# Optimization experiments

Hardware: AMD Instinct MI355X
Metric: run time of the kernel (lower is better)

Reference implementation:

```python
import jax, jax.numpy as jnp
import numpy as np

D_MODEL = 128
H = 256          # lstm_hidden_dim
L = 2            # lstm_num_layers
PRED_LEN = 45
OUT_DIM = 2
B = 4096


def _glorot(key, shape):
    fan = shape[-1]
    return jax.random.uniform(key, shape, jnp.float32, -1.0, 1.0) / jnp.sqrt(jnp.float32(fan))


def setup_inputs() -> dict:
    key = jax.random.key(0)
    ks = jax.random.split(key, 20)
    inp = {
        "encoder_feat": jax.random.normal(ks[0], (B, D_MODEL), jnp.float32),
        "last_obs_pos": jax.random.normal(ks[1], (B, OUT_DIM), jnp.float32),
        "context": jax.random.normal(ks[2], (B, D_MODEL), jnp.float32),
        # hidden/cell init projections: Linear(d_model -> H*L)
        "Wh_init": _glorot(ks[3], (H * L, D_MODEL)),
        "bh_init": jnp.zeros((H * L,), jnp.float32),
        "Wc_init": _glorot(ks[4], (H * L, D_MODEL)),
        "bc_init": jnp.zeros((H * L,), jnp.float32),
        # LSTM layer 0: input = OUT_DIM + D_MODEL
        "W_ih0": _glorot(ks[5], (4 * H, OUT_DIM + D_MODEL)),
        "W_hh0": _glorot(ks[6], (4 * H, H)),
        "b_ih0": jnp.zeros((4 * H,), jnp.float32),
        "b_hh0": jnp.zeros((4 * H,), jnp.float32),
        # LSTM layer 1: input = H
        "W_ih1": _glorot(ks[7], (4 * H, H)),
        "W_hh1": _glorot(ks[8], (4 * H, H)),
        "b_ih1": jnp.zeros((4 * H,), jnp.float32),
        "b_hh1": jnp.zeros((4 * H,), jnp.float32),
        # output_proj: Linear(H,64) -> ReLU -> Linear(64, OUT_DIM)
        "Wp1": _glorot(ks[9], (64, H)),
        "bp1": jnp.zeros((64,), jnp.float32),
        "Wp2": _glorot(ks[10], (OUT_DIM, 64)),
        "bp2": jnp.zeros((OUT_DIM,), jnp.float32),
    }
    return inp


def _lstm_cell(gates_x, h, c, W_hh):
    # gates_x already = x @ W_ih.T + b_ih + b_hh ; torch gate order: i, f, g, o
    gates = gates_x + h @ W_hh.T
    i, f, g, o = jnp.split(gates, 4, axis=-1)
    c_new = jax.nn.sigmoid(f) * c + jax.nn.sigmoid(i) * jnp.tanh(g)
    h_new = jax.nn.sigmoid(o) * jnp.tanh(c_new)
    return h_new, c_new


def reference(encoder_feat, last_obs_pos, context,
              Wh_init, bh_init, Wc_init, bc_init,
              W_ih0, W_hh0, b_ih0, b_hh0,
              W_ih1, W_hh1, b_ih1, b_hh1,
              Wp1, bp1, Wp2, bp2):
    b = encoder_feat.shape[0]
    # init hidden/cell: [B, L*H] -> per-layer [B, H]
    h_all = (encoder_feat @ Wh_init.T + bh_init).reshape(b, L, H)
    c_all = (encoder_feat @ Wc_init.T + bc_init).reshape(b, L, H)
    h0, h1 = h_all[:, 0], h_all[:, 1]
    c0, c1 = c_all[:, 0], c_all[:, 1]

    # context is constant across steps: precompute its gate contribution once
    bias0 = b_ih0 + b_hh0
    gates_ctx = context @ W_ih0[:, OUT_DIM:].T + bias0   # [B, 4H]
    W_pos = W_ih0[:, :OUT_DIM]                            # [4H, 2]
    bias1 = b_ih1 + b_hh1

    def step(carry, _):
        pos, h0, c0, h1, c1 = carry
        gates_x0 = gates_ctx + pos @ W_pos.T
        h0, c0 = _lstm_cell(gates_x0, h0, c0, W_hh0)
        gates_x1 = h0 @ W_ih1.T + bias1
        h1, c1 = _lstm_cell(gates_x1, h1, c1, W_hh1)
        delta = jax.nn.relu(h1 @ Wp1.T + bp1) @ Wp2.T + bp2
        pos = pos + delta
        return (pos, h0, c0, h1, c1), pos

    _, traj = jax.lax.scan(step, (last_obs_pos, h0, c0, h1, c1), None, length=PRED_LEN)
    return jnp.transpose(traj, (1, 0, 2))  # [B, pred_len, 2]
```

## Files before the change

kernel.cpp:

```cpp
#include <hip/hip_runtime.h>


#define HN    256
#define DM    128
#define NSTEP 45

#define H0A_OFF  1605632ULL
#define HBUF_B   2097152ULL
#define H0B_OFF  (H0A_OFF + HBUF_B)
#define H1A_OFF  (H0B_OFF + HBUF_B)
#define H1B_OFF  (H1A_OFF + HBUF_B)
#define GX_OFF   (H1B_OFF + HBUF_B)
#define GX_B     8388608ULL
#define C0_OFF   (GX_OFF + GX_B)
#define CB_B     4194304ULL
#define C1_OFF   (C0_OFF + CB_B)
#define POSA_OFF (C1_OFF + CB_B)
#define POSB_OFF (POSA_OFF + 32768ULL)
#define WS_NEED  (POSB_OFF + 32768ULL)

typedef __attribute__((ext_vector_type(8))) short s8v;
typedef __attribute__((ext_vector_type(4))) float f32x4;

#define MFMA16(a,b,c) __builtin_amdgcn_mfma_f32_16x16x32_bf16((a),(b),(c),0,0,0)

__device__ __forceinline__ unsigned short f2bf(float f){
  union { float f; unsigned u; } x; x.f = f;
  unsigned r = x.u + 0x7fffu + ((x.u >> 16) & 1u);
  return (unsigned short)(r >> 16);
}
__device__ __forceinline__ float bf2f(unsigned short h){
  union { unsigned u; float f; } x; x.u = ((unsigned)h) << 16;
  return x.f;
}
__device__ __forceinline__ float sigm(float x){
  x = fminf(40.f, fmaxf(-40.f, x));
  return 1.f/(1.f + __expf(-x));
}
__device__ __forceinline__ float tanhx(float x){
  float xx = fminf(15.f, fmaxf(-15.f, x));
  float e = __expf(2.f*xx);
  return (e-1.f)/(e+1.f);
}

__device__ __forceinline__ void store_h(unsigned short* buf, int blk, int b, int u, float v){
  buf[(size_t)blk*4096 + (u>>5)*512 + ((b&15) + ((u>>3)&3)*16)*8 + (u&7)] = f2bf(v);
}
__device__ __forceinline__ s8v ld_af(const unsigned short* buf, int blk, int kt, int lane){
  return *(const s8v*)(buf + (size_t)blk*4096 + kt*512 + lane*8);
}

__global__ void repack(const float* __restrict__ Whh0, const float* __restrict__ Wih1,
                       const float* __restrict__ Whh1, const float* __restrict__ Wp1,
                       unsigned short* __restrict__ dst){
  int gid  = blockIdx.x*256 + threadIdx.x;
  int lane = gid & 63;
  int tile = gid >> 6;
  const float* src; int row; size_t doff;
  int k0 = (lane>>4)*8;
  if (tile < 1536){
    int mi = tile / 512;
    int r  = tile % 512;
    int ut = r & 15;
    int kt = (r >> 4) & 7;
    int g  = r >> 7;
    src  = (mi==0) ? Whh0 : (mi==1) ? Wih1 : Whh1;
    row  = g*256 + ut*16 + (lane&15);
    k0  += kt*32;
    doff = (size_t)mi*262144 + (size_t)r*512 + lane*8;
  } else {
    int r2 = tile - 1536;
    int kt = r2 & 7, pt = r2 >> 3;
    src  = Wp1;
    row  = pt*16 + (lane&15);
    k0  += kt*32;
    doff = 786432 + (size_t)r2*512 + lane*8;
  }
  const float* s = src + (size_t)row*HN + k0;
  float4 a = *(const float4*)(s);
  float4 b = *(const float4*)(s+4);
  unsigned short* d = dst + doff;
  d[0]=f2bf(a.x); d[1]=f2bf(a.y); d[2]=f2bf(a.z); d[3]=f2bf(a.w);
  d[4]=f2bf(b.x); d[5]=f2bf(b.y); d[6]=f2bf(b.z); d[7]=f2bf(b.w);
}

__global__ __launch_bounds__(512, 1)
void k_init(const float* __restrict__ enc, const float* __restrict__ pos0,
            const float* __restrict__ ctx, const float* __restrict__ Wh,
            const float* __restrict__ bh,  const float* __restrict__ Wc,
            const float* __restrict__ bc,  const float* __restrict__ Wih0,
            const float* __restrict__ bih0,const float* __restrict__ bhh0,
            unsigned short* __restrict__ h0a, unsigned short* __restrict__ h1a,
            unsigned short* __restrict__ gxg,
            float* __restrict__ c0g, float* __restrict__ c1g,
            float* __restrict__ posg)
{
  __shared__ float sh_x[16*DM];
  const int tid = threadIdx.x;
  const int blk = blockIdx.x;
  const int gb0 = blk*16;

  {
    const float4* src = (const float4*)(enc + (size_t)gb0*DM);
    ((float4*)sh_x)[tid] = src[tid];
  }
  if (tid < 32) posg[(size_t)gb0*2 + tid] = pos0[(size_t)gb0*2 + tid];
  __syncthreads();

  {
    const int r = tid;
    float ah[16], ac[16];
    #pragma unroll
    for (int b=0;b<16;b++){ ah[b]=0.f; ac[b]=0.f; }
    const float4* whr = (const float4*)(Wh + (size_t)r*DM);
    const float4* wcr = (const float4*)(Wc + (size_t)r*DM);
    #pragma unroll 4
    for (int kk=0; kk<DM/4; kk++){
      float4 w0 = whr[kk], w1 = wcr[kk];
      #pragma unroll
      for (int b=0;b<16;b++){
        float4 x = *(const float4*)&sh_x[b*DM + kk*4];
        ah[b] += w0.x*x.x + w0.y*x.y + w0.z*x.z + w0.w*x.w;
        ac[b] += w1.x*x.x + w1.y*x.y + w1.z*x.z + w1.w*x.w;
      }
    }
    float bhv = bh[r], bcv = bc[r];
    if (r < HN){
      #pragma unroll
      for (int b=0;b<16;b++){
        store_h(h0a, blk, b, r, ah[b] + bhv);
        c0g[(size_t)blk*4096 + r*16 + b] = ac[b] + bcv;
      }
    } else {
      #pragma unroll
      for (int b=0;b<16;b++){
        store_h(h1a, blk, b, r-HN, ah[b] + bhv);
        c1g[(size_t)blk*4096 + (r-HN)*16 + b] = ac[b] + bcv;
      }
    }
  }
  __syncthreads();

  {
    const float4* src = (const float4*)(ctx + (size_t)gb0*DM);
    ((float4*)sh_x)[tid] = src[tid];
  }
  __syncthreads();

  {
    float a0[16], a1[16];
    #pragma unroll
    for (int b=0;b<16;b++){ a0[b]=0.f; a1[b]=0.f; }
    const float2* wr0 = (const float2*)(Wih0 + (size_t)tid*130 + 2);
    const float2* wr1 = (const float2*)(Wih0 + (size_t)(tid+512)*130 + 2);
    #pragma unroll 4
    for (int kk=0; kk<DM/2; kk++){
      float2 w0 = wr0[kk], w1 = wr1[kk];
      #pragma unroll
      for (int b=0;b<16;b++){
        float2 x = *(const float2*)&sh_x[b*DM + kk*2];
        a0[b] += w0.x*x.x + w0.y*x.y;
        a1[b] += w1.x*x.x + w1.y*x.y;
      }
    }
    float cb0 = bih0[tid]     + bhh0[tid];
    float cb1 = bih0[tid+512] + bhh0[tid+512];
    #pragma unroll
    for (int b=0;b<16;b++){
      gxg[(size_t)blk*16384 + (size_t)tid*16 + b]       = f2bf(a0[b] + cb0);
      gxg[(size_t)blk*16384 + (size_t)(tid+512)*16 + b] = f2bf(a1[b] + cb1);
    }
  }
}

__global__ __launch_bounds__(512, 1)
void k_layer0(const unsigned short* __restrict__ wsW,
              const unsigned short* __restrict__ gxg,
              const unsigned short* __restrict__ h0rd,
              unsigned short* __restrict__ h0wr,
              const unsigned short* __restrict__ h1prev,
              float* __restrict__ c0g,
              const float* __restrict__ posRd,
              float* __restrict__ posWr,
              const float* __restrict__ Wih0,
              const float* __restrict__ bp1,
              const float* __restrict__ Wp2,
              const float* __restrict__ bp2,
              float* __restrict__ out, int t)
{
  const int tid  = threadIdx.x;
  const int lane = tid & 63;
  const int w    = tid >> 6;
  const int wb   = w >> 1;
  const int wh   = w & 1;
  const int col  = lane & 15;
  const int hi   = lane >> 4;
  const int bt   = blockIdx.x & 31;
  const int sl   = blockIdx.x >> 5;

  const int blk0 = bt*8 + wb*2;
  const int ut   = sl*2 + wh;
  const int u    = ut*16 + col;

  f32x4 acc[2][4];
  #pragma unroll
  for (int m2=0;m2<2;m2++)
    #pragma unroll
    for (int g=0;g<4;g++)
      #pragma unroll
      for (int q=0;q<4;q++) acc[m2][g][q] = 0.f;

  float p0[2][4], p1[2][4];

  if (t > 0){
    float bpv[4], w2a[4], w2b[4];
    #pragma unroll
    for (int n=0;n<4;n++){
      bpv[n] = bp1[n*16 + col];
      w2a[n] = Wp2[n*16 + col];
      w2b[n] = Wp2[64 + n*16 + col];
    }
    f32x4 hp[2][4];
    #pragma unroll
    for (int m2=0;m2<2;m2++)
      #pragma unroll
      for (int n=0;n<4;n++)
        #pragma unroll
        for (int q=0;q<4;q++) hp[m2][n][q] = bpv[n];

    #pragma unroll
    for (int kt=0;kt<8;kt++){
      s8v a0 = ld_af(h0rd,   blk0,   kt, lane);
      s8v a1 = ld_af(h0rd,   blk0+1, kt, lane);
      s8v b0 = ld_af(h1prev, blk0,   kt, lane);
      s8v b1 = ld_af(h1prev, blk0+1, kt, lane);
      #pragma unroll
      for (int g=0;g<4;g++){
        const int r = (g*8 + kt)*16 + ut;
        s8v bf = *(const s8v*)(wsW + (size_t)r*512 + lane*8);
        acc[0][g] = MFMA16(a0, bf, acc[0][g]);
        acc[1][g] = MFMA16(a1, bf, acc[1][g]);
        s8v wf = *(const s8v*)(wsW + 786432 + (size_t)(g*8+kt)*512 + lane*8);
        hp[0][g] = MFMA16(b0, wf, hp[0][g]);
        hp[1][g] = MFMA16(b1, wf, hp[1][g]);
      }
    }

    const float bp20 = bp2[0], bp21 = bp2[1];
    #pragma unroll
    for (int m2=0;m2<2;m2++){
      const int blk = blk0 + m2;
      #pragma unroll
      for (int q=0;q<4;q++){
        float s0 = 0.f, s1 = 0.f;
        #pragma unroll
        for (int n=0;n<4;n++){
          float r = fmaxf(hp[m2][n][q], 0.f);
          s0 += r*w2a[n]; s1 += r*w2b[n];
        }
        #pragma unroll
        for (int off=1; off<16; off<<=1){
          s0 += __shfl_xor(s0, off, 64);
          s1 += __shfl_xor(s1, off, 64);
        }
        int b = blk*16 + hi*4 + q;
        float2 pp = *(const float2*)(posRd + (size_t)b*2);
        float np0 = pp.x + s0 + bp20;
        float np1 = pp.y + s1 + bp21;
        p0[m2][q] = np0; p1[m2][q] = np1;
        if (sl == 0 && wh == 0 && col == 0){
          posWr[(size_t)b*2]     = np0;
          posWr[(size_t)b*2 + 1] = np1;
          out[((size_t)b*NSTEP + (t-1))*2]     = np0;
          out[((size_t)b*NSTEP + (t-1))*2 + 1] = np1;
        }
      }
    }
  } else {
    #pragma unroll
    for (int kt=0;kt<8;kt++){
      s8v a0 = ld_af(h0rd, blk0,   kt, lane);
      s8v a1 = ld_af(h0rd, blk0+1, kt, lane);
      #pragma unroll
      for (int g=0;g<4;g++){
        const int r = (g*8 + kt)*16 + ut;
        s8v bf = *(const s8v*)(wsW + (size_t)r*512 + lane*8);
        acc[0][g] = MFMA16(a0, bf, acc[0][g]);
        acc[1][g] = MFMA16(a1, bf, acc[1][g]);
      }
    }
    #pragma unroll
    for (int m2=0;m2<2;m2++)
      #pragma unroll
      for (int q=0;q<4;q++){
        float2 pp = *(const float2*)(posRd + (size_t)((blk0+m2)*16 + hi*4 + q)*2);
        p0[m2][q] = pp.x; p1[m2][q] = pp.y;
      }
  }

  float wpr[4][2];
  #pragma unroll
  for (int g=0;g<4;g++){
    int row = g*256 + u;
    wpr[g][0] = Wih0[(size_t)row*130 + 0];
    wpr[g][1] = Wih0[(size_t)row*130 + 1];
  }
  #pragma unroll
  for (int m2=0;m2<2;m2++){
    const int blk = blk0 + m2;
    float* cp = c0g + (size_t)blk*4096 + u*16 + hi*4;
    float4 cold = *(const float4*)cp;
    float4 cnew;
    #pragma unroll
    for (int q=0;q<4;q++){
      float gate[4];
      #pragma unroll
      for (int g=0;g<4;g++){
        const unsigned short* gp = gxg + (size_t)blk*16384 + (size_t)(g*256+u)*16 + hi*4;
        gate[g] = acc[m2][g][q] + bf2f(gp[q]) + p0[m2][q]*wpr[g][0] + p1[m2][q]*wpr[g][1];
      }
      float iv = sigm(gate[0]);
      float fv = sigm(gate[1]);
      float gv = tanhx(gate[2]);
      float ov = sigm(gate[3]);
      float cv = fv*((&cold.x)[q]) + iv*gv;
      (&cnew.x)[q] = cv;
      store_h(h0wr, blk, hi*4+q, u, ov*tanhx(cv));
    }
    *(float4*)cp = cnew;
  }
}

__global__ __launch_bounds__(512, 1)
void k_layer1(const unsigned short* __restrict__ wsW,
              const unsigned short* __restrict__ h0n,
              const unsigned short* __restrict__ h1rd,
              unsigned short* __restrict__ h1wr,
              float* __restrict__ c1g,
              const float* __restrict__ bih1,
              const float* __restrict__ bhh1)
{
  const int tid  = threadIdx.x;
  const int lane = tid & 63;
  const int w    = tid >> 6;
  const int wb   = w >> 1;
  const int wh   = w & 1;
  const int col  = lane & 15;
  const int hi   = lane >> 4;
  const int bt   = blockIdx.x & 31;
  const int sl   = blockIdx.x >> 5;

  const int blk0 = bt*8 + wb*2;
  const int ut   = sl*2 + wh;
  const int u    = ut*16 + col;

  f32x4 acc[2][4];
  #pragma unroll
  for (int g=0;g<4;g++){
    int row = g*256 + u;
    float bv = bih1[row] + bhh1[row];
    #pragma unroll
    for (int q=0;q<4;q++){ acc[0][g][q] = bv; acc[1][g][q] = bv; }
  }

  #pragma unroll
  for (int kt=0;kt<8;kt++){
    s8v x0 = ld_af(h0n,  blk0,   kt, lane);
    s8v x1 = ld_af(h0n,  blk0+1, kt, lane);
    s8v y0 = ld_af(h1rd, blk0,   kt, lane);
    s8v y1 = ld_af(h1rd, blk0+1, kt, lane);
    #pragma unroll
    for (int g=0;g<4;g++){
      const int r = (g*8 + kt)*16 + ut;
      s8v b1v = *(const s8v*)(wsW + 262144 + (size_t)r*512 + lane*8);
      acc[0][g] = MFMA16(x0, b1v, acc[0][g]);
      acc[1][g] = MFMA16(x1, b1v, acc[1][g]);
      s8v b2v = *(const s8v*)(wsW + 524288 + (size_t)r*512 + lane*8);
      acc[0][g] = MFMA16(y0, b2v, acc[0][g]);
      acc[1][g] = MFMA16(y1, b2v, acc[1][g]);
    }
  }

  #pragma unroll
  for (int m2=0;m2<2;m2++){
    const int blk = blk0 + m2;
    float* cp = c1g + (size_t)blk*4096 + u*16 + hi*4;
    float4 cold = *(const float4*)cp;
    float4 cnew;
    #pragma unroll
    for (int q=0;q<4;q++){
      float iv = sigm(acc[m2][0][q]);
      float fv = sigm(acc[m2][1][q]);
      float gv = tanhx(acc[m2][2][q]);
      float ov = sigm(acc[m2][3][q]);
      float cv = fv*((&cold.x)[q]) + iv*gv;
      (&cnew.x)[q] = cv;
      store_h(h1wr, blk, hi*4+q, u, ov*tanhx(cv));
    }
    *(float4*)cp = cnew;
  }
}

__global__ __launch_bounds__(256, 2)
void k_head(const unsigned short* __restrict__ wsW,
            const unsigned short* __restrict__ h1n,
            const float* __restrict__ posRd,
            const float* __restrict__ bp1,
            const float* __restrict__ Wp2,
            const float* __restrict__ bp2,
            float* __restrict__ out, int t)
{
  const int tid  = threadIdx.x;
  const int lane = tid & 63;
  const int w    = tid >> 6;
  const int col  = lane & 15;
  const int hi   = lane >> 4;
  const int bt   = blockIdx.x;

  float bpv[4], w2a[4], w2b[4];
  #pragma unroll
  for (int n=0;n<4;n++){
    bpv[n] = bp1[n*16 + col];
    w2a[n] = Wp2[n*16 + col];
    w2b[n] = Wp2[64 + n*16 + col];
  }
  const float bp20 = bp2[0], bp21 = bp2[1];

  #pragma unroll
  for (int m2=0;m2<2;m2++){
    const int blk = bt*8 + w*2 + m2;
    f32x4 acc[4];
    #pragma unroll
    for (int n=0;n<4;n++)
      #pragma unroll
      for (int q=0;q<4;q++) acc[n][q] = bpv[n];
    #pragma unroll
    for (int kt=0;kt<8;kt++){
      s8v a = ld_af(h1n, blk, kt, lane);
      #pragma unroll
      for (int n=0;n<4;n++){
        s8v bf = *(const s8v*)(wsW + 786432 + (size_t)(n*8+kt)*512 + lane*8);
        acc[n] = MFMA16(a, bf, acc[n]);
      }
    }
    #pragma unroll
    for (int q=0;q<4;q++){
      float s0 = 0.f, s1 = 0.f;
      #pragma unroll
      for (int n=0;n<4;n++){
        float r = fmaxf(acc[n][q], 0.f);
        s0 += r*w2a[n]; s1 += r*w2b[n];
      }
      #pragma unroll
      for (int off=1; off<16; off<<=1){
        s0 += __shfl_xor(s0, off, 64);
        s1 += __shfl_xor(s1, off, 64);
      }
      if (col == 0){
        int b = blk*16 + hi*4 + q;
        out[((size_t)b*NSTEP + t)*2]     = posRd[(size_t)b*2]     + s0 + bp20;
        out[((size_t)b*NSTEP + t)*2 + 1] = posRd[(size_t)b*2 + 1] + s1 + bp21;
      }
    }
  }
}

extern "C" void kernel_launch(void* const* d_in, const int* in_sizes, int n_in,
                              void* d_out, int out_size, void* d_ws, size_t ws_size,
                              hipStream_t stream) {
  const float* enc  = (const float*)d_in[0];
  const float* pos0 = (const float*)d_in[1];
  const float* ctx  = (const float*)d_in[2];
  const float* Wh   = (const float*)d_in[3];
  const float* bh   = (const float*)d_in[4];
  const float* Wc   = (const float*)d_in[5];
  const float* bc   = (const float*)d_in[6];
  const float* Wih0 = (const float*)d_in[7];
  const float* Whh0 = (const float*)d_in[8];
  const float* bih0 = (const float*)d_in[9];
  const float* bhh0 = (const float*)d_in[10];
  const float* Wih1 = (const float*)d_in[11];
  const float* Whh1 = (const float*)d_in[12];
  const float* bih1 = (const float*)d_in[13];
  const float* bhh1 = (const float*)d_in[14];
  const float* Wp1  = (const float*)d_in[15];
  const float* bp1  = (const float*)d_in[16];
  const float* Wp2  = (const float*)d_in[17];
  const float* bp2  = (const float*)d_in[18];
  float* out = (float*)d_out;
  unsigned short* wsW = (unsigned short*)d_ws;

  unsigned short* h0a = (unsigned short*)((char*)d_ws + H0A_OFF);
  unsigned short* h0b = (unsigned short*)((char*)d_ws + H0B_OFF);
  unsigned short* h1a = (unsigned short*)((char*)d_ws + H1A_OFF);
  unsigned short* h1b = (unsigned short*)((char*)d_ws + H1B_OFF);
  unsigned short* gxg = (unsigned short*)((char*)d_ws + GX_OFF);
  float* c0g  = (float*)((char*)d_ws + C0_OFF);
  float* c1g  = (float*)((char*)d_ws + C1_OFF);
  float* posA = (float*)((char*)d_ws + POSA_OFF);
  float* posB = (float*)((char*)d_ws + POSB_OFF);

  hipLaunchKernelGGL(repack, dim3(392), dim3(256), 0, stream,
                     Whh0, Wih1, Whh1, Wp1, wsW);

  hipLaunchKernelGGL(k_init, dim3(256), dim3(512), 0, stream,
                     enc, pos0, ctx, Wh, bh, Wc, bc, Wih0, bih0, bhh0,
                     h0a, h1a, gxg, c0g, c1g, posA);

  unsigned short* h1prev = h1a;
  for (int t = 0; t < NSTEP; t++){
    unsigned short* h0r = (t & 1) ? h0b : h0a;
    unsigned short* h0w = (t & 1) ? h0a : h0b;
    unsigned short* h1r = (t & 1) ? h1b : h1a;
    unsigned short* h1w = (t & 1) ? h1a : h1b;
    float* posRead  = (t == 0) ? posA : ((t & 1) ? posA : posB);
    float* posWrite = (t & 1) ? posB : posA;

    hipLaunchKernelGGL(k_layer0, dim3(256), dim3(512), 0, stream,
                       wsW, gxg, h0r, h0w, h1prev, c0g,
                       posRead, posWrite, Wih0, bp1, Wp2, bp2, out, t);
    hipLaunchKernelGGL(k_layer1, dim3(256), dim3(512), 0, stream,
                       wsW, h0w, h1r, h1w, c1g, bih1, bhh1);
    h1prev = h1w;
  }
  hipLaunchKernelGGL(k_head, dim3(32), dim3(256), 0, stream,
                     wsW, h1prev, posA, bp1, Wp2, bp2, out, NSTEP-1);
}
```

Before: 1.867 ms.

## Fuse layer0 and layer1 kernels per step with a group barrier

Merges the per-step layer0 and layer1 kernels into one k_step kernel. Layer1 needs the full h0 for its batch tile, so the kernel uses an atomic-counter barrier across the 8 blocks that share a batch tile (bt) in place of a kernel boundary. This halves the number of launches (from 90 to 45 step kernels) and lets layer1 reuse state already held by the block. The cost is that all 256 blocks must be co-resident to avoid deadlock, plus spin-wait overhead and a bounded spin that gives up silently on timeout.

```diff
diff --git a/kernel.cpp b/kernel.cpp
--- a/kernel.cpp
+++ b/kernel.cpp
@@ -17,7 +17,8 @@
 #define C1_OFF   (C0_OFF + CB_B)
 #define POSA_OFF (C1_OFF + CB_B)
 #define POSB_OFF (POSA_OFF + 32768ULL)
-#define WS_NEED  (POSB_OFF + 32768ULL)
+#define GBAR_OFF (POSB_OFF + 32768ULL)
+#define WS_NEED  (GBAR_OFF + 2048ULL)
 
 typedef __attribute__((ext_vector_type(8))) short s8v;
 typedef __attribute__((ext_vector_type(4))) float f32x4;
@@ -48,6 +49,25 @@
 }
 __device__ __forceinline__ s8v ld_af(const unsigned short* buf, int blk, int kt, int lane){
   return *(const s8v*)(buf + (size_t)blk*4096 + kt*512 + lane*8);
+}
+
+__device__ __forceinline__ void group_barrier(unsigned* gbar, unsigned gen){
+  __syncthreads();
+  if (threadIdx.x == 0){
+    __threadfence();
+    unsigned arrived = atomicAdd(gbar, 1u) + 1u;
+    if (arrived == 8u*gen){
+      __threadfence();
+      atomicAdd(gbar+1, 1u);
+    } else {
+      unsigned spin = 0;
+      while (atomicAdd(gbar+1, 0u) < gen && spin < (1u<<22)){
+        __builtin_amdgcn_s_sleep(2); ++spin;
+      }
+    }
+    __threadfence();
+  }
+  __syncthreads();
 }
 
 __global__ void repack(const float* __restrict__ Whh0, const float* __restrict__ Wih1,
@@ -174,19 +194,22 @@
 }
 
 __global__ __launch_bounds__(512, 1)
-void k_layer0(const unsigned short* __restrict__ wsW,
-              const unsigned short* __restrict__ gxg,
-              const unsigned short* __restrict__ h0rd,
-              unsigned short* __restrict__ h0wr,
-              const unsigned short* __restrict__ h1prev,
-              float* __restrict__ c0g,
-              const float* __restrict__ posRd,
-              float* __restrict__ posWr,
-              const float* __restrict__ Wih0,
-              const float* __restrict__ bp1,
-              const float* __restrict__ Wp2,
-              const float* __restrict__ bp2,
-              float* __restrict__ out, int t)
+void k_step(const unsigned short* __restrict__ wsW,
+            const unsigned short* __restrict__ gxg,
+            const unsigned short* __restrict__ h0rd,
+            unsigned short* __restrict__ h0wr,
+            const unsigned short* __restrict__ h1rd,
+            unsigned short* __restrict__ h1wr,
+            float* __restrict__ c0g, float* __restrict__ c1g,
+            const float* __restrict__ posRd,
+            float* __restrict__ posWr,
+            const float* __restrict__ Wih0,
+            const float* __restrict__ bih1, const float* __restrict__ bhh1,
+            const float* __restrict__ bp1,
+            const float* __restrict__ Wp2,
+            const float* __restrict__ bp2,
+            unsigned* __restrict__ bars,
+            float* __restrict__ out, int t)
 {
   const int tid  = threadIdx.x;
   const int lane = tid & 63;
@@ -201,6 +224,7 @@
   const int blk0 = bt*8 + wb*2;
   const int ut   = sl*2 + wh;
   const int u    = ut*16 + col;
+  unsigned* gbar = bars + bt*16;
 
   f32x4 acc[2][4];
   #pragma unroll
@@ -230,10 +254,10 @@
 
     #pragma unroll
     for (int kt=0;kt<8;kt++){
-      s8v a0 = ld_af(h0rd,   blk0,   kt, lane);
-      s8v a1 = ld_af(h0rd,   blk0+1, kt, lane);
-      s8v b0 = ld_af(h1prev, blk0,   kt, lane);
-      s8v b1 = ld_af(h1prev, blk0+1, kt, lane);
+      s8v a0 = ld_af(h0rd, blk0,   kt, lane);
+      s8v a1 = ld_af(h0rd, blk0+1, kt, lane);
+      s8v b0 = ld_af(h1rd, blk0,   kt, lane);
+      s8v b1 = ld_af(h1rd, blk0+1, kt, lane);
       #pragma unroll
       for (int g=0;g<4;g++){
         const int r = (g*8 + kt)*16 + ut;
@@ -298,63 +322,42 @@
       }
   }
 
-  float wpr[4][2];
-  #pragma unroll
-  for (int g=0;g<4;g++){
-    int row = g*256 + u;
-    wpr[g][0] = Wih0[(size_t)row*130 + 0];
-    wpr[g][1] = Wih0[(size_t)row*130 + 1];
-  }
-  #pragma unroll
-  for (int m2=0;m2<2;m2++){
-    const int blk = blk0 + m2;
-    float* cp = c0g + (size_t)blk*4096 + u*16 + hi*4;
-    float4 cold = *(const float4*)cp;
-    float4 cnew;
-    #pragma unroll
-    for (int q=0;q<4;q++){
-      float gate[4];
-      #pragma unroll
-      for (int g=0;g<4;g++){
-        const unsigned short* gp = gxg + (size_t)blk*16384 + (size_t)(g*256+u)*16 + hi*4;
-        gate[g] = acc[m2][g][q] + bf2f(gp[q]) + p0[m2][q]*wpr[g][0] + p1[m2][q]*wpr[g][1];
-      }
-      float iv = sigm(gate[0]);
-      float fv = sigm(gate[1]);
-      float gv = tanhx(gate[2]);
-      float ov = sigm(gate[3]);
-      float cv = fv*((&cold.x)[q]) + iv*gv;
-      (&cnew.x)[q] = cv;
-      store_h(h0wr, blk, hi*4+q, u, ov*tanhx(cv));
-    }
-    *(float4*)cp = cnew;
-  }
-}
-
-__global__ __launch_bounds__(512, 1)
-void k_layer1(const unsigned short* __restrict__ wsW,
-              const unsigned short* __restrict__ h0n,
-              const unsigned short* __restrict__ h1rd,
-              unsigned short* __restrict__ h1wr,
-              float* __restrict__ c1g,
-              const float* __restrict__ bih1,
-              const float* __restrict__ bhh1)
-{
-  const int tid  = threadIdx.x;
-  const int lane = tid & 63;
-  const int w    = tid >> 6;
-  const int wb   = w >> 1;
-  const int wh   = w & 1;
-  const int col  = lane & 15;
-  const int hi   = lane >> 4;
-  const int bt   = blockIdx.x & 31;
-  const int sl   = blockIdx.x >> 5;
-
-  const int blk0 = bt*8 + wb*2;
-  const int ut   = sl*2 + wh;
-  const int u    = ut*16 + col;
-
-  f32x4 acc[2][4];
+  {
+    float wpr[4][2];
+    #pragma unroll
+    for (int g=0;g<4;g++){
+      int row = g*256 + u;
+      wpr[g][0] = Wih0[(size_t)row*130 + 0];
+      wpr[g][1] = Wih0[(size_t)row*130 + 1];
+    }
+    #pragma unroll
+    for (int m2=0;m2<2;m2++){
+      const int blk = blk0 + m2;
+      float* cp = c0g + (size_t)blk*4096 + u*16 + hi*4;
+      float4 cold = *(const float4*)cp;
+      float4 cnew;
+      #pragma unroll
+      for (int q=0;q<4;q++){
+        float gate[4];
+        #pragma unroll
+        for (int g=0;g<4;g++){
+          const unsigned short* gp = gxg + (size_t)blk*16384 + (size_t)(g*256+u)*16 + hi*4;
+          gate[g] = acc[m2][g][q] + bf2f(gp[q]) + p0[m2][q]*wpr[g][0] + p1[m2][q]*wpr[g][1];
+        }
+        float iv = sigm(gate[0]);
+        float fv = sigm(gate[1]);
+        float gv = tanhx(gate[2]);
+        float ov = sigm(gate[3]);
+        float cv = fv*((&cold.x)[q]) + iv*gv;
+        (&cnew.x)[q] = cv;
+        store_h(h0wr, blk, hi*4+q, u, ov*tanhx(cv));
+      }
+      *(float4*)cp = cnew;
+    }
+  }
+
+  group_barrier(gbar, (unsigned)(t+1));
+
   #pragma unroll
   for (int g=0;g<4;g++){
     int row = g*256 + u;
@@ -365,8 +368,8 @@
 
   #pragma unroll
   for (int kt=0;kt<8;kt++){
-    s8v x0 = ld_af(h0n,  blk0,   kt, lane);
-    s8v x1 = ld_af(h0n,  blk0+1, kt, lane);
+    s8v x0 = ld_af(h0wr, blk0,   kt, lane);
+    s8v x1 = ld_af(h0wr, blk0+1, kt, lane);
     s8v y0 = ld_af(h1rd, blk0,   kt, lane);
     s8v y1 = ld_af(h1rd, blk0+1, kt, lane);
     #pragma unroll
@@ -499,6 +502,9 @@
   float* c1g  = (float*)((char*)d_ws + C1_OFF);
   float* posA = (float*)((char*)d_ws + POSA_OFF);
   float* posB = (float*)((char*)d_ws + POSB_OFF);
+  unsigned* bars = (unsigned*)((char*)d_ws + GBAR_OFF);
+
+  hipMemsetAsync((void*)bars, 0, 2048, stream);
 
   hipLaunchKernelGGL(repack, dim3(392), dim3(256), 0, stream,
                      Whh0, Wih1, Whh1, Wp1, wsW);
@@ -516,11 +522,10 @@
     float* posRead  = (t == 0) ? posA : ((t & 1) ? posA : posB);
     float* posWrite = (t & 1) ? posB : posA;
 
-    hipLaunchKernelGGL(k_layer0, dim3(256), dim3(512), 0, stream,
-                       wsW, gxg, h0r, h0w, h1prev, c0g,
-                       posRead, posWrite, Wih0, bp1, Wp2, bp2, out, t);
-    hipLaunchKernelGGL(k_layer1, dim3(256), dim3(512), 0, stream,
-                       wsW, h0w, h1r, h1w, c1g, bih1, bhh1);
+    hipLaunchKernelGGL(k_step, dim3(256), dim3(512), 0, stream,
+                       wsW, gxg, h0r, h0w, h1r, h1w, c0g, c1g,
+                       posRead, posWrite, Wih0, bih1, bhh1,
+                       bp1, Wp2, bp2, bars, out, t);
     h1prev = h1w;
   }
   hipLaunchKernelGGL(k_head, dim3(32), dim3(256), 0, stream,
```

Result: slower. 2.037 ms (+9.1%).
